# Kernel optimization log

Hardware: AMD Instinct MI355X
Metric: run time of the kernel (lower is better)

Reference implementation:

```python
import jax, jax.numpy as jnp
import numpy as np
import math

D_MODEL = 1024
N_HEADS = 16
D_HEAD = D_MODEL // N_HEADS
EPS = 1e-5


def layer_norm(x, w, b):
    mu = jnp.mean(x, axis=-1, keepdims=True)
    var = jnp.mean(jnp.square(x - mu), axis=-1, keepdims=True)
    return (x - mu) * jax.lax.rsqrt(var + EPS) * w + b


def setup_inputs() -> dict:
    key = jax.random.key(0)
    ks = jax.random.split(key, 8)
    b, n, d = 1, 4096, D_MODEL
    s = 0.02
    return {
        "x": jax.random.normal(ks[0], (b, n, d), dtype=jnp.float32),
        "ln1_w": jnp.ones((d,), jnp.float32),
        "ln1_b": jnp.zeros((d,), jnp.float32),
        "ln2_w": jnp.ones((d,), jnp.float32),
        "ln2_b": jnp.zeros((d,), jnp.float32),
        "w_qkv": jax.random.normal(ks[1], (d, 3 * d), jnp.float32) * s,  # [in, out]
        "w_o": jax.random.normal(ks[2], (d, d), jnp.float32) * s,
        "w_ff1": jax.random.normal(ks[3], (d, 4 * d), jnp.float32) * s,
        "b_ff1": jnp.zeros((4 * d,), jnp.float32),
        "w_ff2": jax.random.normal(ks[4], (4 * d, d), jnp.float32) * s,
        "b_ff2": jnp.zeros((d,), jnp.float32),
    }


def reference(x, ln1_w, ln1_b, ln2_w, ln2_b, w_qkv, w_o, w_ff1, b_ff1, w_ff2, b_ff2):
    b, n, d = x.shape
    # --- attention sub-block ---
    h = layer_norm(x, ln1_w, ln1_b)
    qkv = (h @ w_qkv).reshape(b, n, 3, N_HEADS, D_HEAD)
    q, k, v = qkv[:, :, 0], qkv[:, :, 1], qkv[:, :, 2]  # [b, n, h, dh]
    scale = 1.0 / math.sqrt(D_HEAD)
    s = jnp.einsum("bqhd,bkhd->bhqk", q, k) * scale  # materialized [b,h,n,n]
    causal = jnp.tril(jnp.ones((n, n), dtype=bool))
    s = jnp.where(causal, s, -jnp.inf)
    a = jax.nn.softmax(s, axis=-1)
    out = jnp.einsum("bhqk,bkhd->bqhd", a, v).reshape(b, n, d)
    x = x + out @ w_o
    # --- FFN sub-block ---
    h2 = layer_norm(x, ln2_w, ln2_b)
    ff = jax.nn.gelu(h2 @ w_ff1 + b_ff1, approximate=False) @ w_ff2 + b_ff2
    return x + ff
```

## Files before the change

### kernel.cpp

```cpp
#include <hip/hip_runtime.h>
#include <hip/hip_bf16.h>
#include <cstdint>
#include <cstddef>

typedef __attribute__((ext_vector_type(8))) __bf16 bf16x8;
typedef __attribute__((ext_vector_type(4))) __bf16 bf16x4;
typedef __attribute__((ext_vector_type(4))) float f32x4;
typedef __attribute__((ext_vector_type(16))) float f32x16;
typedef __attribute__((ext_vector_type(4))) unsigned int uint4v;

#define MFMA16(a, b, c) __builtin_amdgcn_mfma_f32_16x16x32_bf16(a, b, c, 0, 0, 0)
#define MFMA32(a, b, c) __builtin_amdgcn_mfma_f32_32x32x16_bf16(a, b, c, 0, 0, 0)

__device__ __forceinline__ void gload_lds16(const void* g, void* l) {
  __builtin_amdgcn_global_load_lds(
      (__attribute__((address_space(1))) uint32_t*)g,
      (__attribute__((address_space(3))) uint32_t*)l,
      16, 0, 0);
}

__device__ __forceinline__ unsigned pkbf(float a, float b) {
  unsigned short x = __builtin_bit_cast(unsigned short, (__bf16)a);
  unsigned short y = __builtin_bit_cast(unsigned short, (__bf16)b);
  return (unsigned)x | ((unsigned)y << 16);
}

__global__ __launch_bounds__(256) void transpose_cvt_kernel(
    const float* __restrict__ in, __bf16* __restrict__ out, int K, int N) {
  __shared__ float tile[32][33];
  int bx = blockIdx.x, by = blockIdx.y;
  int tx = threadIdx.x, ty = threadIdx.y;
  int gcol = bx * 32 + tx;
#pragma unroll
  for (int j = 0; j < 4; j++) {
    int grow = by * 32 + ty + j * 8;
    tile[ty + j * 8][tx] = in[(size_t)grow * N + gcol];
  }
  __syncthreads();
#pragma unroll
  for (int j = 0; j < 4; j++) {
    int n = bx * 32 + ty + j * 8;
    out[(size_t)n * K + by * 32 + tx] = (__bf16)tile[tx][ty + j * 8];
  }
}

__global__ __launch_bounds__(256) void ln_kernel(
    const float* __restrict__ x, const float* __restrict__ w,
    const float* __restrict__ b, __bf16* __restrict__ out) {
  int row = blockIdx.x;
  int t = threadIdx.x;
  const float4* xr = (const float4*)(x + (size_t)row * 1024);
  float4 v = xr[t];
  float s = v.x + v.y + v.z + v.w;
  float sq = v.x * v.x + v.y * v.y + v.z * v.z + v.w * v.w;
#pragma unroll
  for (int m = 1; m < 64; m <<= 1) {
    s += __shfl_xor(s, m);
    sq += __shfl_xor(sq, m);
  }
  __shared__ float rs[4], rq[4];
  int wid = t >> 6;
  if ((t & 63) == 0) { rs[wid] = s; rq[wid] = sq; }
  __syncthreads();
  s = rs[0] + rs[1] + rs[2] + rs[3];
  sq = rq[0] + rq[1] + rq[2] + rq[3];
  float mean = s * (1.0f / 1024.0f);
  float var = sq * (1.0f / 1024.0f) - mean * mean;
  float rstd = rsqrtf(var + 1e-5f);
  int c = t * 4;
  float4 wv = ((const float4*)w)[t];
  float4 bv = ((const float4*)b)[t];
  bf16x4 o;
  o[0] = (__bf16)((v.x - mean) * rstd * wv.x + bv.x);
  o[1] = (__bf16)((v.y - mean) * rstd * wv.y + bv.y);
  o[2] = (__bf16)((v.z - mean) * rstd * wv.z + bv.z);
  o[3] = (__bf16)((v.w - mean) * rstd * wv.w + bv.w);
  *(bf16x4*)(out + (size_t)row * 1024 + c) = o;
}

template <int EPI>
__global__ __launch_bounds__(256, 2) void gemm_kernel(
    const __bf16* __restrict__ A, const __bf16* __restrict__ BT,
    int M, int N, int K,
    const float* __restrict__ resid, const float* __restrict__ bias,
    float* __restrict__ outf, __bf16* __restrict__ outb) {
  __shared__ __bf16 lsA[128 * 64];
  __shared__ __bf16 lsB[128 * 64];
  int t = threadIdx.x;
  int m0 = blockIdx.y * 128, n0 = blockIdx.x * 128;
  int wid = t >> 6, lane = t & 63, lo = lane & 15, g = lane >> 4;
  int wr = wid >> 1, wc = wid & 1;
  f32x4 acc[4][4] = {};
  const __bf16* ag = A + (size_t)(m0 + (t >> 3)) * K + (t & 7) * 8;
  const __bf16* bg = BT + (size_t)(n0 + (t >> 3)) * K + (t & 7) * 8;
  for (int k0 = 0; k0 < K; k0 += 64) {
#pragma unroll
    for (int i = 0; i < 4; i++) {
      gload_lds16(ag + (size_t)i * 32 * K + k0, &lsA[i * 2048 + t * 8]);
      gload_lds16(bg + (size_t)i * 32 * K + k0, &lsB[i * 2048 + t * 8]);
    }
    __syncthreads();
#pragma unroll
    for (int kk = 0; kk < 2; kk++) {
      bf16x8 af[4], bfr[4];
#pragma unroll
      for (int mi = 0; mi < 4; mi++)
        af[mi] = *(const bf16x8*)&lsA[(wr * 64 + mi * 16 + lo) * 64 + kk * 32 + g * 8];
#pragma unroll
      for (int ni = 0; ni < 4; ni++)
        bfr[ni] = *(const bf16x8*)&lsB[(wc * 64 + ni * 16 + lo) * 64 + kk * 32 + g * 8];
#pragma unroll
      for (int mi = 0; mi < 4; mi++)
#pragma unroll
        for (int ni = 0; ni < 4; ni++)
          acc[mi][ni] = MFMA16(af[mi], bfr[ni], acc[mi][ni]);
    }
    __syncthreads();
  }
#pragma unroll
  for (int mi = 0; mi < 4; mi++) {
#pragma unroll
    for (int ni = 0; ni < 4; ni++) {
      int col = n0 + wc * 64 + ni * 16 + lo;
      int row0 = m0 + wr * 64 + mi * 16 + g * 4;
#pragma unroll
      for (int r = 0; r < 4; r++) {
        int row = row0 + r;
        float val = acc[mi][ni][r];
        size_t idx = (size_t)row * N + col;
        outf[idx] = resid[idx] + val;
      }
    }
  }
}

template <int EPI>
__global__ __launch_bounds__(512, 2) void gemm256_kernel(
    const __bf16* __restrict__ A, const __bf16* __restrict__ BT,
    int M, int N, int K, int nkc,
    const float* __restrict__ bias, __bf16* __restrict__ outb,
    __bf16* __restrict__ P0, __bf16* __restrict__ P1,
    __bf16* __restrict__ P2, __bf16* __restrict__ P3) {
  __shared__ __bf16 lsA[2][2][128 * 64];
  __shared__ __bf16 lsB[2][2][128 * 64];
  int nbx = N >> 8;
  int nwg = (M >> 8) * nbx;
  int bid = blockIdx.x;
  int swz = (bid & 7) * (nwg >> 3) + (bid >> 3);
  int m0 = (swz / nbx) << 8, n0 = (swz % nbx) << 8;
  int kc = blockIdx.y;
  int kt0 = kc * nkc;
  int t = threadIdx.x;
  int wid = t >> 6, lane = t & 63, lo = lane & 15, g = lane >> 4;
  int wm = wid >> 2, wn = wid & 3;
  int srow = t >> 3, sgrp = t & 7;

  auto stA = [&](int d, int h, int kt) {
#pragma unroll
    for (int i = 0; i < 2; i++) {
      int row = i * 64 + srow;
      int gs = (sgrp ^ (row & 7)) * 8;
      gload_lds16(A + (size_t)(m0 + h * 128 + row) * K + kt * 64 + gs,
                  &lsA[d][h][(i * 512 + t) * 8]);
    }
  };
  auto stB = [&](int d, int h, int kt) {
#pragma unroll
    for (int i = 0; i < 2; i++) {
      int row = i * 64 + srow;
      int gs = (sgrp ^ (row & 7)) * 8;
      gload_lds16(BT + (size_t)(n0 + h * 128 + row) * K + kt * 64 + gs,
                  &lsB[d][h][(i * 512 + t) * 8]);
    }
  };
  auto rdA = [&](int d, int f, int kk) -> bf16x8 {
    int row = (f & 3) * 32 + wm * 16 + lo;
    return *(const bf16x8*)&lsA[d][f >> 2][row * 64 + (((kk * 4 + g) ^ (lo & 7)) * 8)];
  };
  auto rdB = [&](int d, int ni, int kk) -> bf16x8 {
    int row = (ni & 1) * 64 + wn * 16 + lo;
    return *(const bf16x8*)&lsB[d][ni >> 1][row * 64 + (((kk * 4 + g) ^ (lo & 7)) * 8)];
  };

  f32x4 acc[8][4] = {};
  stA(0, 0, kt0); stB(0, 0, kt0); stB(0, 1, kt0); stA(0, 1, kt0);
  asm volatile("s_waitcnt vmcnt(4)" ::: "memory");
  __builtin_amdgcn_s_barrier();

  for (int ki = 0; ki < nkc; ki++) {
    int kt = kt0 + ki;
    int d = ki & 1, nx = d ^ 1;
    bool pf = (ki + 1) < nkc;
    bf16x8 fa[4][2], fb0[2][2], fb1[2][2];
#pragma unroll
    for (int f = 0; f < 4; f++) { fa[f][0] = rdA(d, f, 0); fa[f][1] = rdA(d, f, 1); }
#pragma unroll
    for (int n = 0; n < 2; n++) { fb0[n][0] = rdB(d, n, 0); fb0[n][1] = rdB(d, n, 1); }
    if (pf) { stA(nx, 0, kt + 1); stB(nx, 0, kt + 1); }
    __builtin_amdgcn_s_barrier();
    __builtin_amdgcn_s_setprio(1);
#pragma unroll
    for (int f = 0; f < 4; f++)
#pragma unroll
      for (int n = 0; n < 2; n++) {
        acc[f][n] = MFMA16(fa[f][0], fb0[n][0], acc[f][n]);
        acc[f][n] = MFMA16(fa[f][1], fb0[n][1], acc[f][n]);
      }
    __builtin_amdgcn_s_setprio(0);
    asm volatile("s_waitcnt vmcnt(6)" ::: "memory");
    __builtin_amdgcn_s_barrier();
#pragma unroll
    for (int n = 0; n < 2; n++) { fb1[n][0] = rdB(d, 2 + n, 0); fb1[n][1] = rdB(d, 2 + n, 1); }
    if (pf) stB(nx, 1, kt + 1);
    __builtin_amdgcn_s_barrier();
    __builtin_amdgcn_s_setprio(1);
#pragma unroll
    for (int f = 0; f < 4; f++)
#pragma unroll
      for (int n = 0; n < 2; n++) {
        acc[f][2 + n] = MFMA16(fa[f][0], fb1[n][0], acc[f][2 + n]);
        acc[f][2 + n] = MFMA16(fa[f][1], fb1[n][1], acc[f][2 + n]);
      }
    __builtin_amdgcn_s_setprio(0);
    asm volatile("s_waitcnt vmcnt(6)" ::: "memory");
    __builtin_amdgcn_s_barrier();
#pragma unroll
    for (int f = 0; f < 4; f++) { fa[f][0] = rdA(d, 4 + f, 0); fa[f][1] = rdA(d, 4 + f, 1); }
    if (pf) stA(nx, 1, kt + 1);
    __builtin_amdgcn_s_barrier();
    __builtin_amdgcn_s_setprio(1);
#pragma unroll
    for (int f = 0; f < 4; f++)
#pragma unroll
      for (int n = 0; n < 2; n++) {
        acc[4 + f][2 + n] = MFMA16(fa[f][0], fb1[n][0], acc[4 + f][2 + n]);
        acc[4 + f][2 + n] = MFMA16(fa[f][1], fb1[n][1], acc[4 + f][2 + n]);
      }
    __builtin_amdgcn_s_setprio(0);
    __builtin_amdgcn_s_barrier();
    __builtin_amdgcn_s_setprio(1);
#pragma unroll
    for (int f = 0; f < 4; f++)
#pragma unroll
      for (int n = 0; n < 2; n++) {
        acc[4 + f][n] = MFMA16(fa[f][0], fb0[n][0], acc[4 + f][n]);
        acc[4 + f][n] = MFMA16(fa[f][1], fb0[n][1], acc[4 + f][n]);
      }
    __builtin_amdgcn_s_setprio(0);
    asm volatile("s_waitcnt vmcnt(4)" ::: "memory");
    __builtin_amdgcn_s_barrier();
  }

  __bf16* pk = (EPI == 4) ? ((kc == 0) ? P0 : (kc == 1) ? P1 : (kc == 2) ? P2 : P3)
                          : nullptr;
#pragma unroll
  for (int f = 0; f < 8; f++) {
    int row0 = m0 + (f >> 2) * 128 + (f & 3) * 32 + wm * 16 + g * 4;
#pragma unroll
    for (int ni = 0; ni < 4; ni++) {
      int col = n0 + (ni >> 1) * 128 + (ni & 1) * 64 + wn * 16 + lo;
      if (EPI == 0) {
        int sE = col >> 10, rem = col & 1023, hh = rem >> 6, dd = rem & 63;
        if (sE < 2) {
          float qs = (sE == 0) ? 0.1803368801111204f : 1.0f;
#pragma unroll
          for (int r = 0; r < 4; r++)
            outb[((size_t)(sE * 16 + hh) * 4096 + row0 + r) * 64 + dd] =
                (__bf16)(acc[f][ni][r] * qs);
        } else {
          bf16x4 pk4;
#pragma unroll
          for (int r = 0; r < 4; r++) pk4[r] = (__bf16)acc[f][ni][r];
          *(bf16x4*)&outb[(size_t)32 * 4096 * 64 + ((size_t)(hh * 64 + dd)) * 4096 + row0] = pk4;
        }
      } else if (EPI == 2) {
        float bv = bias[col];
#pragma unroll
        for (int r = 0; r < 4; r++) {
          float vv = acc[f][ni][r] + bv;
          float gg = 0.5f * vv * (1.0f + erff(vv * 0.70710678118f));
          outb[(size_t)(row0 + r) * N + col] = (__bf16)gg;
        }
      } else {
#pragma unroll
        for (int r = 0; r < 4; r++)
          pk[(size_t)(row0 + r) * N + col] = (__bf16)acc[f][ni][r];
      }
    }
  }
}

__global__ __launch_bounds__(256) void ff2_reduce_kernel(
    const __bf16* __restrict__ p0, const __bf16* __restrict__ p1,
    const __bf16* __restrict__ p2, const __bf16* __restrict__ p3,
    const float* __restrict__ x2, const float* __restrict__ bias,
    float* __restrict__ out) {
  size_t i8 = ((size_t)blockIdx.x * 256 + threadIdx.x) * 8;
  bf16x8 a = *(const bf16x8*)&p0[i8];
  bf16x8 b = *(const bf16x8*)&p1[i8];
  bf16x8 c = *(const bf16x8*)&p2[i8];
  bf16x8 d = *(const bf16x8*)&p3[i8];
  int col = (int)(i8 & 1023);
  float4 xa = *(const float4*)&x2[i8];
  float4 xb = *(const float4*)&x2[i8 + 4];
  float4 ba = *(const float4*)&bias[col];
  float4 bb = *(const float4*)&bias[col + 4];
  float4 oa, ob;
  oa.x = xa.x + ba.x + (float)a[0] + (float)b[0] + (float)c[0] + (float)d[0];
  oa.y = xa.y + ba.y + (float)a[1] + (float)b[1] + (float)c[1] + (float)d[1];
  oa.z = xa.z + ba.z + (float)a[2] + (float)b[2] + (float)c[2] + (float)d[2];
  oa.w = xa.w + ba.w + (float)a[3] + (float)b[3] + (float)c[3] + (float)d[3];
  ob.x = xb.x + bb.x + (float)a[4] + (float)b[4] + (float)c[4] + (float)d[4];
  ob.y = xb.y + bb.y + (float)a[5] + (float)b[5] + (float)c[5] + (float)d[5];
  ob.z = xb.z + bb.z + (float)a[6] + (float)b[6] + (float)c[6] + (float)d[6];
  ob.w = xb.w + bb.w + (float)a[7] + (float)b[7] + (float)c[7] + (float)d[7];
  *(float4*)&out[i8] = oa;
  *(float4*)&out[i8 + 4] = ob;
}

__global__ __launch_bounds__(512, 4) void attn_kernel(
    const __bf16* __restrict__ Q, const __bf16* __restrict__ Kb,
    const __bf16* __restrict__ VTb, __bf16* __restrict__ O) {
  constexpr int NSEQ = 4096;
  __shared__ __bf16 lds[2][2][2][64 * 64];
  int orig = blockIdx.x;
  int xcd = orig & 7, rank = orig >> 3;
  int hv = rank >> 5;
  int hd2 = (rank >> 4) & 1;
  int itr = rank & 15;
  int head = xcd * 2 + hd2;
  int it = hv ? itr : (31 - itr);
  int t = threadIdx.x, wid = t >> 6, lane = t & 63;
  int lo = lane & 31, hi = lane >> 5;
  int qsub = wid & 3, kpar = wid >> 2;
  const __bf16* kh = Kb + (size_t)head * NSEQ * 64;
  const __bf16* vth = VTb + (size_t)head * 64 * NSEQ;
  int qlow = it * 128 + qsub * 32;
  int qrow = qlow + lo;
  const __bf16* qh = Q + (size_t)head * NSEQ * 64 + (size_t)qrow * 64;
  bf16x8 bq[4];
#pragma unroll
  for (int c = 0; c < 4; c++) bq[c] = *(const bf16x8*)(qh + c * 16 + hi * 8);

  f32x16 acc0 = {}, acc1 = {};
  float l = 0.f;
  int srow = t >> 3;
  int sgs = ((t & 7) ^ (srow & 7)) * 8;

  auto stage_tile = [&](int d, int par, int kt) {
    gload_lds16(kh + (size_t)(kt * 64 + srow) * 64 + sgs, &lds[d][par][0][t * 8]);
    gload_lds16(vth + (size_t)srow * NSEQ + kt * 64 + sgs, &lds[d][par][1][t * 8]);
  };

  int ns = it + 1;
  stage_tile(0, 0, 0);
  stage_tile(0, 1, 1);
  __syncthreads();
  for (int j = 0; j < ns; j++) {
    int cur = j & 1;
    if (j + 1 < ns) {
      stage_tile(cur ^ 1, 0, 2 * j + 2);
      stage_tile(cur ^ 1, 1, 2 * j + 3);
    }
    int kt = 2 * j + kpar;
    if (kt * 64 <= qlow + 31) {
      const __bf16* lk = lds[cur][kpar][0];
      const __bf16* lvt = lds[cur][kpar][1];
      f32x16 s0 = {}, s1 = {};
      __builtin_amdgcn_s_setprio(1);
#pragma unroll
      for (int c = 0; c < 4; c++) {
        bf16x8 ka0 = *(const bf16x8*)&lk[(size_t)lo * 64 + (((c * 2 + hi) ^ (lo & 7)) * 8)];
        bf16x8 ka1 = *(const bf16x8*)&lk[(size_t)(32 + lo) * 64 + (((c * 2 + hi) ^ (lo & 7)) * 8)];
        s0 = MFMA32(ka0, bq[c], s0);
        s1 = MFMA32(ka1, bq[c], s1);
      }
      __builtin_amdgcn_s_setprio(0);
      float sv[32];
#pragma unroll
      for (int i = 0; i < 16; i++) { sv[i] = s0[i]; sv[16 + i] = s1[i]; }
      if (kt * 64 + 63 > qlow) {
#pragma unroll
        for (int i = 0; i < 32; i++) {
          int r = i & 15, kc = i >> 4;
          int key = kt * 64 + kc * 32 + (r & 3) + 8 * (r >> 2) + 4 * hi;
          if (key > qrow) sv[i] = -3.0e38f;
        }
      }
      float ps0 = 0, ps1 = 0, ps2 = 0, ps3 = 0;
#pragma unroll
      for (int i = 0; i < 32; i += 4) {
        sv[i] = exp2f(sv[i]);         ps0 += sv[i];
        sv[i + 1] = exp2f(sv[i + 1]); ps1 += sv[i + 1];
        sv[i + 2] = exp2f(sv[i + 2]); ps2 += sv[i + 2];
        sv[i + 3] = exp2f(sv[i + 3]); ps3 += sv[i + 3];
      }
      l += (ps0 + ps1) + (ps2 + ps3);
      uint4v pw[4];
#pragma unroll
      for (int b = 0; b < 4; b++) {
        int off = b * 8;
        unsigned a0 = pkbf(sv[off + 0], sv[off + 1]);
        unsigned a1 = pkbf(sv[off + 2], sv[off + 3]);
        unsigned b0 = pkbf(sv[off + 4], sv[off + 5]);
        unsigned b1 = pkbf(sv[off + 6], sv[off + 7]);
        asm("v_permlane32_swap_b32 %0, %1" : "+v"(a0), "+v"(b0));
        asm("v_permlane32_swap_b32 %0, %1" : "+v"(a1), "+v"(b1));
        pw[b][0] = a0; pw[b][1] = a1; pw[b][2] = b0; pw[b][3] = b1;
      }
      __builtin_amdgcn_s_setprio(1);
#pragma unroll
      for (int b = 0; b < 4; b++) {
        bf16x8 pf = __builtin_bit_cast(bf16x8, pw[b]);
        bf16x8 va0 = *(const bf16x8*)&lvt[(size_t)lo * 64 + (((b * 2 + hi) ^ (lo & 7)) * 8)];
        bf16x8 va1 = *(const bf16x8*)&lvt[(size_t)(32 + lo) * 64 + (((b * 2 + hi) ^ (lo & 7)) * 8)];
        acc0 = MFMA32(va0, pf, acc0);
        acc1 = MFMA32(va1, pf, acc1);
      }
      __builtin_amdgcn_s_setprio(0);
    }
    __syncthreads();
  }
  float* fl = (float*)lds;
  float* lbuf = fl;
  float* ab = fl + 256;
  __bf16* bounce = (__bf16*)(fl + 256 + 9216);
  if (kpar == 1) {
    lbuf[qsub * 64 + lane] = l;
    int base = (qsub * 64 + lane) * 36;
#pragma unroll
    for (int k2 = 0; k2 < 16; k2 += 4) {
      float4 v0; v0.x = acc0[k2]; v0.y = acc0[k2 + 1]; v0.z = acc0[k2 + 2]; v0.w = acc0[k2 + 3];
      *(float4*)&ab[base + k2] = v0;
      float4 v1; v1.x = acc1[k2]; v1.y = acc1[k2 + 1]; v1.z = acc1[k2 + 2]; v1.w = acc1[k2 + 3];
      *(float4*)&ab[base + 16 + k2] = v1;
    }
  }
  __syncthreads();
  if (kpar == 0) {
    float lsum = l + lbuf[qsub * 64 + lane];
    lsum += __shfl_xor(lsum, 32);
    float linv = 1.0f / lsum;
    int base = (qsub * 64 + lane) * 36;
    f32x16 b0, b1;
#pragma unroll
    for (int k2 = 0; k2 < 16; k2 += 4) {
      float4 v0 = *(float4*)&ab[base + k2];
      b0[k2] = v0.x; b0[k2 + 1] = v0.y; b0[k2 + 2] = v0.z; b0[k2 + 3] = v0.w;
      float4 v1 = *(float4*)&ab[base + 16 + k2];
      b1[k2] = v1.x; b1[k2 + 1] = v1.y; b1[k2 + 2] = v1.z; b1[k2 + 3] = v1.w;
    }
    __bf16* region = bounce + qsub * 2048;
#pragma unroll
    for (int dt = 0; dt < 2; dt++) {
#pragma unroll
      for (int rp = 0; rp < 8; rp++) {
        int r = rp * 2;
        float a0 = dt ? acc1[r] : acc0[r], a1 = dt ? acc1[r + 1] : acc0[r + 1];
        float c0 = dt ? b1[r] : b0[r], c1 = dt ? b1[r + 1] : b0[r + 1];
        float e0 = (a0 + c0) * linv;
        float e1 = (a1 + c1) * linv;
        int d = dt * 32 + (r & 3) + 8 * (r >> 2) + 4 * hi;
        int bytecol = d * 2;
        int g16 = bytecol >> 4, rem16 = bytecol & 15;
        *(unsigned*)((char*)region + lo * 128 + ((g16 ^ (lo & 7)) * 16 + rem16)) = pkbf(e0, e1);
      }
    }
#pragma unroll
    for (int j2 = 0; j2 < 4; j2++) {
      int idx = j2 * 64 + lane;
      int row = idx >> 3, g = idx & 7;
      bf16x8 v = *(const bf16x8*)((char*)region + row * 128 + ((g ^ (row & 7)) * 16));
      *(bf16x8*)&O[(size_t)(it * 128 + qsub * 32 + row) * 1024 + head * 64 + g * 8] = v;
    }
  }
}

extern "C" void kernel_launch(void* const* d_in, const int* in_sizes, int n_in,
                              void* d_out, int out_size, void* d_ws, size_t ws_size,
                              hipStream_t stream) {
  const float* x = (const float*)d_in[0];
  const float* ln1_w = (const float*)d_in[1];
  const float* ln1_b = (const float*)d_in[2];
  const float* ln2_w = (const float*)d_in[3];
  const float* ln2_b = (const float*)d_in[4];
  const float* w_qkv = (const float*)d_in[5];
  const float* w_o = (const float*)d_in[6];
  const float* w_ff1 = (const float*)d_in[7];
  const float* b_ff1 = (const float*)d_in[8];
  const float* w_ff2 = (const float*)d_in[9];
  const float* b_ff2 = (const float*)d_in[10];
  float* out = (float*)d_out;

  const size_t D = 1024, NT = 4096;
  __bf16* wqkvT = (__bf16*)d_ws;
  __bf16* woT = wqkvT + 3072 * D;
  __bf16* wff1T = woT + D * D;
  __bf16* wff2T = wff1T + 4096 * D;
  __bf16* hbuf = wff2T + D * 4096;
  __bf16* qkvb = hbuf + NT * D;
  __bf16* attnb = qkvb + 3 * NT * D;
  __bf16* a1 = qkvb;
  float* x2 = (float*)(attnb + NT * D);
  __bf16* p0 = (__bf16*)d_ws;
  __bf16* p1 = p0 + NT * D;
  __bf16* p2 = hbuf;
  __bf16* p3 = (__bf16*)(x2 + NT * D);

  dim3 tb(32, 8);
  transpose_cvt_kernel<<<dim3(3072 / 32, 1024 / 32), tb, 0, stream>>>(w_qkv, wqkvT, 1024, 3072);
  transpose_cvt_kernel<<<dim3(1024 / 32, 1024 / 32), tb, 0, stream>>>(w_o, woT, 1024, 1024);
  transpose_cvt_kernel<<<dim3(4096 / 32, 1024 / 32), tb, 0, stream>>>(w_ff1, wff1T, 1024, 4096);
  transpose_cvt_kernel<<<dim3(1024 / 32, 4096 / 32), tb, 0, stream>>>(w_ff2, wff2T, 4096, 1024);

  ln_kernel<<<4096, 256, 0, stream>>>(x, ln1_w, ln1_b, hbuf);
  gemm256_kernel<0><<<192, 512, 0, stream>>>(hbuf, wqkvT, 4096, 3072, 1024, 16,
                                             nullptr, qkvb, nullptr, nullptr, nullptr, nullptr);
  attn_kernel<<<512, 512, 0, stream>>>(
      qkvb, qkvb + 16 * NT * 64, qkvb + 32 * NT * 64, attnb);
  gemm_kernel<1><<<dim3(1024 / 128, 4096 / 128), 256, 0, stream>>>(
      attnb, woT, 4096, 1024, 1024, x, nullptr, x2, nullptr);
  ln_kernel<<<4096, 256, 0, stream>>>(x2, ln2_w, ln2_b, hbuf);
  gemm256_kernel<2><<<256, 512, 0, stream>>>(hbuf, wff1T, 4096, 4096, 1024, 16,
                                             b_ff1, a1, nullptr, nullptr, nullptr, nullptr);
  gemm256_kernel<4><<<dim3(64, 4), 512, 0, stream>>>(a1, wff2T, 4096, 1024, 4096, 16,
                                                     nullptr, nullptr, p0, p1, p2, p3);
  ff2_reduce_kernel<<<2048, 256, 0, stream>>>(p0, p1, p2, p3, x2, b_ff2, out);
}
```

Before: 253.3 us.

## Merge weight transposes into one launch and compute softmax row sums via MFMA

```diff
diff --git a/kernel.cpp b/kernel.cpp
--- a/kernel.cpp
+++ b/kernel.cpp
@@ -25,10 +25,18 @@
   return (unsigned)x | ((unsigned)y << 16);
 }
 
-__global__ __launch_bounds__(256) void transpose_cvt_kernel(
-    const float* __restrict__ in, __bf16* __restrict__ out, int K, int N) {
+__global__ __launch_bounds__(256) void transpose_all_kernel(
+    const float* __restrict__ w_qkv, __bf16* __restrict__ wqkvT,
+    const float* __restrict__ w_o, __bf16* __restrict__ woT,
+    const float* __restrict__ w_ff1, __bf16* __restrict__ wff1T,
+    const float* __restrict__ w_ff2, __bf16* __restrict__ wff2T) {
   __shared__ float tile[32][33];
-  int bx = blockIdx.x, by = blockIdx.y;
+  int bid = blockIdx.x;
+  const float* in; __bf16* out; int K, N, bx, by;
+  if (bid < 3072)      { in = w_qkv; out = wqkvT; K = 1024; N = 3072; bx = bid % 96;  by = bid / 96; }
+  else if (bid < 4096) { int b = bid - 3072; in = w_o;   out = woT;   K = 1024; N = 1024; bx = b % 32;  by = b / 32; }
+  else if (bid < 8192) { int b = bid - 4096; in = w_ff1; out = wff1T; K = 1024; N = 4096; bx = b % 128; by = b / 128; }
+  else                 { int b = bid - 8192; in = w_ff2; out = wff2T; K = 4096; N = 1024; bx = b % 32;  by = b / 32; }
   int tx = threadIdx.x, ty = threadIdx.y;
   int gcol = bx * 32 + tx;
 #pragma unroll
@@ -342,8 +350,12 @@
 #pragma unroll
   for (int c = 0; c < 4; c++) bq[c] = *(const bf16x8*)(qh + c * 16 + hi * 8);
 
+  const unsigned onesu = 0x3F803F80u;
+  uint4v onev = {onesu, onesu, onesu, onesu};
+  bf16x8 vones = __builtin_bit_cast(bf16x8, onev);
+
   f32x16 acc0 = {}, acc1 = {};
-  float l = 0.f;
+  f32x16 lacc = {};
   int srow = t >> 3;
   int sgs = ((t & 7) ^ (srow & 7)) * 8;
 
@@ -376,37 +388,37 @@
         s1 = MFMA32(ka1, bq[c], s1);
       }
       __builtin_amdgcn_s_setprio(0);
-      float sv[32];
-#pragma unroll
-      for (int i = 0; i < 16; i++) { sv[i] = s0[i]; sv[16 + i] = s1[i]; }
       if (kt * 64 + 63 > qlow) {
 #pragma unroll
-        for (int i = 0; i < 32; i++) {
-          int r = i & 15, kc = i >> 4;
-          int key = kt * 64 + kc * 32 + (r & 3) + 8 * (r >> 2) + 4 * hi;
-          if (key > qrow) sv[i] = -3.0e38f;
+        for (int i = 0; i < 16; i++) {
+          int key0 = kt * 64 + (i & 3) + 8 * (i >> 2) + 4 * hi;
+          if (key0 > qrow) s0[i] = -3.0e38f;
+          if (key0 + 32 > qrow) s1[i] = -3.0e38f;
         }
       }
-      float ps0 = 0, ps1 = 0, ps2 = 0, ps3 = 0;
-#pragma unroll
-      for (int i = 0; i < 32; i += 4) {
-        sv[i] = exp2f(sv[i]);         ps0 += sv[i];
-        sv[i + 1] = exp2f(sv[i + 1]); ps1 += sv[i + 1];
-        sv[i + 2] = exp2f(sv[i + 2]); ps2 += sv[i + 2];
-        sv[i + 3] = exp2f(sv[i + 3]); ps3 += sv[i + 3];
-      }
-      l += (ps0 + ps1) + (ps2 + ps3);
+#pragma unroll
+      for (int i = 0; i < 16; i++) {
+        s0[i] = exp2f(s0[i]);
+        s1[i] = exp2f(s1[i]);
+      }
       uint4v pw[4];
 #pragma unroll
-      for (int b = 0; b < 4; b++) {
+      for (int b = 0; b < 2; b++) {
         int off = b * 8;
-        unsigned a0 = pkbf(sv[off + 0], sv[off + 1]);
-        unsigned a1 = pkbf(sv[off + 2], sv[off + 3]);
-        unsigned b0 = pkbf(sv[off + 4], sv[off + 5]);
-        unsigned b1 = pkbf(sv[off + 6], sv[off + 7]);
+        unsigned a0 = pkbf(s0[off + 0], s0[off + 1]);
+        unsigned a1 = pkbf(s0[off + 2], s0[off + 3]);
+        unsigned b0 = pkbf(s0[off + 4], s0[off + 5]);
+        unsigned b1 = pkbf(s0[off + 6], s0[off + 7]);
         asm("v_permlane32_swap_b32 %0, %1" : "+v"(a0), "+v"(b0));
         asm("v_permlane32_swap_b32 %0, %1" : "+v"(a1), "+v"(b1));
         pw[b][0] = a0; pw[b][1] = a1; pw[b][2] = b0; pw[b][3] = b1;
+        unsigned c0 = pkbf(s1[off + 0], s1[off + 1]);
+        unsigned c1 = pkbf(s1[off + 2], s1[off + 3]);
+        unsigned d0 = pkbf(s1[off + 4], s1[off + 5]);
+        unsigned d1 = pkbf(s1[off + 6], s1[off + 7]);
+        asm("v_permlane32_swap_b32 %0, %1" : "+v"(c0), "+v"(d0));
+        asm("v_permlane32_swap_b32 %0, %1" : "+v"(c1), "+v"(d1));
+        pw[2 + b][0] = c0; pw[2 + b][1] = c1; pw[2 + b][2] = d0; pw[2 + b][3] = d1;
       }
       __builtin_amdgcn_s_setprio(1);
 #pragma unroll
@@ -416,6 +428,7 @@
         bf16x8 va1 = *(const bf16x8*)&lvt[(size_t)(32 + lo) * 64 + (((b * 2 + hi) ^ (lo & 7)) * 8)];
         acc0 = MFMA32(va0, pf, acc0);
         acc1 = MFMA32(va1, pf, acc1);
+        lacc = MFMA32(vones, pf, lacc);
       }
       __builtin_amdgcn_s_setprio(0);
     }
@@ -426,7 +439,7 @@
   float* ab = fl + 256;
   __bf16* bounce = (__bf16*)(fl + 256 + 9216);
   if (kpar == 1) {
-    lbuf[qsub * 64 + lane] = l;
+    lbuf[qsub * 64 + lane] = lacc[0];
     int base = (qsub * 64 + lane) * 36;
 #pragma unroll
     for (int k2 = 0; k2 < 16; k2 += 4) {
@@ -438,8 +451,7 @@
   }
   __syncthreads();
   if (kpar == 0) {
-    float lsum = l + lbuf[qsub * 64 + lane];
-    lsum += __shfl_xor(lsum, 32);
+    float lsum = lacc[0] + lbuf[qsub * 64 + lane];
     float linv = 1.0f / lsum;
     int base = (qsub * 64 + lane) * 36;
     f32x16 b0, b1;
@@ -508,10 +520,8 @@
   __bf16* p3 = (__bf16*)(x2 + NT * D);
 
   dim3 tb(32, 8);
-  transpose_cvt_kernel<<<dim3(3072 / 32, 1024 / 32), tb, 0, stream>>>(w_qkv, wqkvT, 1024, 3072);
-  transpose_cvt_kernel<<<dim3(1024 / 32, 1024 / 32), tb, 0, stream>>>(w_o, woT, 1024, 1024);
-  transpose_cvt_kernel<<<dim3(4096 / 32, 1024 / 32), tb, 0, stream>>>(w_ff1, wff1T, 1024, 4096);
-  transpose_cvt_kernel<<<dim3(1024 / 32, 4096 / 32), tb, 0, stream>>>(w_ff2, wff2T, 4096, 1024);
+  transpose_all_kernel<<<12288, tb, 0, stream>>>(w_qkv, wqkvT, w_o, woT,
+                                                 w_ff1, wff1T, w_ff2, wff2T);
 
   ln_kernel<<<4096, 256, 0, stream>>>(x, ln1_w, ln1_b, hbuf);
   gemm256_kernel<0><<<192, 512, 0, stream>>>(hbuf, wqkvT, 4096, 3072, 1024, 16,
```

Measured after the change: 247.8 us. 1.02x faster.
